# Performance work log

Measured on AMD Instinct MI355X. Metric: run time of the kernel, lower is better.

Reference implementation:

```python
import jax, jax.numpy as jnp
import numpy as np
from jax import lax

N_ROIS = 1024
ROI_H, ROI_W = 112, 224   # height divisible by 7; band = 16 rows
BANDS = 7
POOL_H, POOL_W = 8, 16    # adaptive max pool target
CONF_THRES = 0.25
PROV, ALPHA, AD = 38, 25, 35
FLAT = 16 * (POOL_H // 2) * (POOL_W // 2)  # 512 after conv+2x2 maxpool


def setup_inputs() -> dict:
    key = jax.random.key(0)
    ks = jax.random.split(key, 16)
    x = jax.random.normal(ks[0], (1, 3, 1024, 1024), dtype=jnp.float32)
    x1 = jax.random.randint(ks[1], (N_ROIS,), 0, 1024 - ROI_W)
    y1 = jax.random.randint(ks[2], (N_ROIS,), 0, 1024 - ROI_H)
    rois = jnp.stack([x1, y1, x1 + ROI_W, y1 + ROI_H], axis=-1).astype(jnp.int32)
    detection_targets = jax.random.randint(ks[3], (N_ROIS,), 0, PROV).astype(jnp.int32)
    classification_targets = jax.random.randint(ks[4], (N_ROIS, 8), 0, ALPHA).astype(jnp.int32)
    conv_w = jax.random.normal(ks[5], (16, 3, 3, 3), dtype=jnp.float32) * 0.1
    conv_b = jnp.zeros((16,), dtype=jnp.float32)
    w1 = jax.random.normal(ks[6], (8, FLAT, 128), dtype=jnp.float32) * 0.05
    b1 = jnp.zeros((8, 128), dtype=jnp.float32)
    w2_prov = jax.random.normal(ks[7], (128, PROV), dtype=jnp.float32) * 0.05
    b2_prov = jnp.zeros((PROV,), dtype=jnp.float32)
    w2_alpha = jax.random.normal(ks[8], (128, ALPHA), dtype=jnp.float32) * 0.05
    b2_alpha = jnp.zeros((ALPHA,), dtype=jnp.float32)
    w2_ad = jax.random.normal(ks[9], (6, 128, AD), dtype=jnp.float32) * 0.05
    b2_ad = jnp.zeros((6, AD), dtype=jnp.float32)
    return dict(x=x, rois=rois, detection_targets=detection_targets,
                classification_targets=classification_targets,
                conv_w=conv_w, conv_b=conv_b, w1=w1, b1=b1,
                w2_prov=w2_prov, b2_prov=b2_prov,
                w2_alpha=w2_alpha, b2_alpha=b2_alpha,
                w2_ad=w2_ad, b2_ad=b2_ad)


def _ce(logits, tgt):
    # per-row cross entropy; matches nn.CrossEntropyLoss on batch of 1 (mean==single)
    lp = jax.nn.log_softmax(logits, axis=-1)
    return -jnp.take_along_axis(lp, tgt[:, None], axis=1)[:, 0]


def _forward(x, rois, detection_targets, classification_targets,
             conv_w, conv_b, w1, b1, w2_prov, b2_prov,
             w2_alpha, b2_alpha, w2_ad, b2_ad):
    n = rois.shape[0]
    m = n * BANDS

    def extract(roi):
        return lax.dynamic_slice(x[0], (0, roi[1], roi[0]), (3, ROI_H, ROI_W))

    crops = jax.vmap(extract)(rois)                       # (N,3,112,224)
    band_h = ROI_H // BANDS                                # 16
    sub = crops.reshape(n, 3, BANDS, band_h, ROI_W)
    sub = sub.transpose(0, 2, 1, 3, 4).reshape(m, 3, band_h, ROI_W)  # (M,3,16,224)
    # adaptive max pool (16,224) -> (8,16): exact 2x14 windows
    pooled = sub.reshape(m, 3, POOL_H, band_h // POOL_H, POOL_W, ROI_W // POOL_W).max(axis=(3, 5))

    feat = lax.conv_general_dilated(pooled, conv_w, (1, 1), 'SAME',
                                    dimension_numbers=('NCHW', 'OIHW', 'NCHW'))
    feat = jax.nn.relu(feat + conv_b[None, :, None, None])  # (M,16,8,16)
    feat = feat.reshape(m, 16, POOL_H // 2, 2, POOL_W // 2, 2).max(axis=(3, 5))  # (M,16,4,8)
    flat = feat.reshape(m, FLAT)                             # (M,512)

    h = jax.nn.relu(jnp.einsum('md,kdh->kmh', flat, w1) + b1[:, None, :])  # (8,M,128)
    out_prov = h[0] @ w2_prov + b2_prov                      # (M,38)
    out_alpha = h[1] @ w2_alpha + b2_alpha                   # (M,25)
    out_ad = jnp.einsum('kmh,khc->kmc', h[2:], w2_ad) + b2_ad[:, None, :]  # (6,M,35)

    det_t = jnp.repeat(detection_targets, BANDS)             # (M,)
    det_loss = _ce(out_prov, det_t)
    mask = det_loss < CONF_THRES

    cls_t = jnp.repeat(classification_targets, BANDS, axis=0)  # (M,8)
    cls_loss = _ce(out_prov, cls_t[:, 0]) + _ce(out_alpha, cls_t[:, 1])
    cls_loss = cls_loss + jax.vmap(_ce)(out_ad, cls_t[:, 2:].T).sum(axis=0)
    total = jnp.sum(jnp.where(mask, cls_loss, 0.0))
    return out_prov, out_alpha, out_ad, mask, total


def reference(x, rois, detection_targets, classification_targets,
              conv_w, conv_b, w1, b1, w2_prov, b2_prov,
              w2_alpha, b2_alpha, w2_ad, b2_ad):
    return _forward(x, rois, detection_targets, classification_targets,
                    conv_w, conv_b, w1, b1, w2_prov, b2_prov,
                    w2_alpha, b2_alpha, w2_ad, b2_ad)
```

## Files before the change

kernel.cpp:

```cpp
#include <hip/hip_runtime.h>

#define NROIS 1024
#define BANDS 7
#define M_TOT (NROIS*BANDS)
#define ROI_W 224
#define BAND_H 16
#define FLATD 512
#define HD 1024
#define PROV 38
#define ALPHA 25
#define ADC 35
#define NAD 6

#define OFF_A     (M_TOT*PROV)
#define OFF_AD    (OFF_A + M_TOT*ALPHA)
#define OFF_MASK  (OFF_AD + NAD*M_TOT*ADC)
#define OFF_TOTAL (OFF_MASK + M_TOT)

typedef __attribute__((ext_vector_type(4))) float f32x4;
typedef __attribute__((ext_vector_type(8))) short bf16x8;

static __device__ __forceinline__ unsigned short f2bf(float f){
    union { float f; unsigned int u; } v; v.f = f;
    unsigned int u = v.u;
    unsigned int r = (u + 0x7fffu + ((u >> 16) & 1u)) >> 16;
    return (unsigned short)r;
}

#define GL16(gp, lp) __builtin_amdgcn_global_load_lds( \
    (const __attribute__((address_space(1))) unsigned int*)(gp), \
    (__attribute__((address_space(3))) unsigned int*)(lp), 16, 0, 0)

#define P2ROW(c,row) (((size_t)((c)*1023 + (row)))*1022)

__global__ __launch_bounds__(256) void k_pre_cvt(
    const float* __restrict__ x, const float* __restrict__ w1,
    const float* __restrict__ w2p, const float* __restrict__ b2p,
    const float* __restrict__ w2a, const float* __restrict__ b2a,
    const float* __restrict__ w2ad, const float* __restrict__ b2ad,
    float* __restrict__ P, unsigned short* __restrict__ Bt,
    unsigned short* __restrict__ B2, float* __restrict__ bias2)
{
    __shared__ float v[1024];
    int blk = blockIdx.x;
    int t = threadIdx.x;
    if (blk < 3069){
        int c = blk / 1023, r = blk - c*1023;
        const float* row0 = x + ((size_t)c*1024 + r)*1024;
        const float* row1 = row0 + 1024;
        #pragma unroll
        for (int i=0;i<4;i++){
            int j = t + i*256;
            v[j] = fmaxf(row0[j], row1[j]);
        }
        __syncthreads();
        float* Pr = P + P2ROW(c, r);
        #pragma unroll
        for (int i=0;i<4;i++){
            int o = t + i*256;
            if (o < 1022){
                int s = o / 73, q = o - s*73;
                int j = 14*q + s;
                if (j < 1011){
                    float mv = v[j];
                    #pragma unroll
                    for (int d=1;d<14;d++) mv = fmaxf(mv, v[j+d]);
                    Pr[o] = mv;
                }
            }
        }
    } else {
        int i = (blk - 3069)*256 + t;
        if (i < 524288){
            int k = i >> 10, n = i & 1023;
            float val = w1[((size_t)(n>>7)*512 + k)*128 + (n&127)];
            Bt[(size_t)n*512 + k] = f2bf(val);
        } else {
            int j = i - 524288;
            int h = j / 6144;
            int rem = j - h*6144;
            int n = rem >> 7, k = rem & 127;
            float val = 0.f;
            if (h == 0){ if (n < 38) val = w2p[k*38 + n]; }
            else if (h == 1){ if (n < 25) val = w2a[k*25 + n]; }
            else { if (n < 35) val = w2ad[(size_t)(h-2)*128*35 + k*35 + n]; }
            B2[j] = f2bf(val);
            if (j < 8*48){
                int hh = j / 48, nn = j - hh*48;
                float bv = 0.f;
                if (hh == 0){ if (nn < 38) bv = b2p[nn]; }
                else if (hh == 1){ if (nn < 25) bv = b2a[nn]; }
                else { if (nn < 35) bv = b2ad[(hh-2)*35 + nn]; }
                bias2[j] = bv;
            }
        }
    }
}

__global__ __launch_bounds__(256) void k_extract(
    const float* __restrict__ P, const int* __restrict__ rois,
    const float* __restrict__ conv_w, const float* __restrict__ conv_b,
    unsigned short* __restrict__ flat)
{
    __shared__ float pl[3][10][19];
    __shared__ float cw[432];
    __shared__ float cb[16];

    int blk = blockIdx.x;
    int r = blk / BANDS, b = blk - r*BANDS;
    int xx = rois[r*4+0];
    int yy = rois[r*4+1] + b*BAND_H;
    int t = threadIdx.x;
    int sx = xx % 14, qx = xx / 14;

    for (int i=t;i<432;i+=256) cw[i]=conv_w[i];
    if (t<16) cb[t]=conv_b[t];
    for (int i=t;i<3*10*19;i+=256) ((float*)pl)[i]=0.f;
    __syncthreads();

    for (int idx=t; idx<384; idx+=256){
        int c = idx>>7; int rem = idx&127; int ph = rem>>4; int pw = rem&15;
        pl[c][ph+1][pw+1] = P[P2ROW(c, yy + 2*ph) + (size_t)sx*73 + qx + pw];
    }
    __syncthreads();

    #pragma unroll
    for (int pass=0; pass<2; pass++){
        int f = t + pass*256;
        int o = f>>5, p=(f>>3)&3, q=f&7;
        float bias = cb[o];
        float s00=bias, s01=bias, s10=bias, s11=bias;
        #pragma unroll
        for (int c=0;c<3;c++){
            float w[9];
            #pragma unroll
            for (int k=0;k<9;k++) w[k] = cw[(o*3+c)*9 + k];
            float pt[4][4];
            #pragma unroll
            for (int di=0; di<4; di++)
              #pragma unroll
              for (int dj=0; dj<4; dj++)
                pt[di][dj] = pl[c][2*p+di][2*q+dj];
            #pragma unroll
            for (int kh=0;kh<3;kh++)
              #pragma unroll
              for (int kw=0;kw<3;kw++){
                float ww = w[kh*3+kw];
                s00 += pt[kh  ][kw  ]*ww;
                s01 += pt[kh  ][kw+1]*ww;
                s10 += pt[kh+1][kw  ]*ww;
                s11 += pt[kh+1][kw+1]*ww;
              }
        }
        float mx = fmaxf(fmaxf(fmaxf(s00,s01), fmaxf(s10,s11)), 0.f);
        flat[(size_t)blk*512 + f] = f2bf(mx);
    }
}

__global__ __launch_bounds__(256) void k_fc1_heads(
    const unsigned short* __restrict__ A, const unsigned short* __restrict__ Bt,
    const float* __restrict__ b1, const unsigned short* __restrict__ B2,
    const float* __restrict__ bias2, float* __restrict__ out,
    float* __restrict__ lse_ws)
{
    __shared__ short smem[16896];
    short* As = smem;
    short* Bs = smem + 8192;
    short* Hl = smem;

    int bm = blockIdx.x, h = blockIdx.y;
    int m0 = bm*128;
    int t = threadIdx.x;
    int wid = t >> 6, lane = t & 63;
    int wr = wid >> 1, wc = wid & 1;
    int l15 = lane & 15, l4 = lane >> 4;

    if (bm == 0 && h == 0 && t == 0) out[OFF_TOTAL] = 0.f;

    const unsigned short* gA = A  + ((size_t)(m0    + wid*16 + (lane>>2)))*FLATD + (lane&3)*8;
    const unsigned short* gB = Bt + ((size_t)(h*128 + wid*16 + (lane>>2)))*FLATD + (lane&3)*8;

    f32x4 acc[4][4];
    #pragma unroll
    for (int i=0;i<4;i++)
      #pragma unroll
      for (int j=0;j<4;j++) acc[i][j] = (f32x4){0.f,0.f,0.f,0.f};

    GL16(gA,            As + wid*512);
    GL16(gA + 64*FLATD, As + 2048 + wid*512);
    GL16(gB,            Bs + wid*512);
    GL16(gB + 64*FLATD, Bs + 2048 + wid*512);
    __syncthreads();

    #pragma unroll
    for (int ks=0; ks<16; ks++){
        int cur = ks & 1;
        if (ks < 15){
            int k1 = (ks+1)*32;
            int nb = (cur^1)*4096;
            GL16(gA + k1,            As + nb + wid*512);
            GL16(gA + 64*FLATD + k1, As + nb + 2048 + wid*512);
            GL16(gB + k1,            Bs + nb + wid*512);
            GL16(gB + 64*FLATD + k1, Bs + nb + 2048 + wid*512);
        }
        bf16x8 af[4], bfv[4];
        #pragma unroll
        for (int mf=0;mf<4;mf++) af[mf]  = *(const bf16x8*)&As[cur*4096 + (wr*64 + mf*16 + l15)*32 + l4*8];
        #pragma unroll
        for (int nf=0;nf<4;nf++) bfv[nf] = *(const bf16x8*)&Bs[cur*4096 + (wc*64 + nf*16 + l15)*32 + l4*8];
        #pragma unroll
        for (int mf=0;mf<4;mf++)
          #pragma unroll
          for (int nf=0;nf<4;nf++)
            acc[mf][nf] = __builtin_amdgcn_mfma_f32_16x16x32_bf16(af[mf], bfv[nf], acc[mf][nf], 0, 0, 0);
        __syncthreads();
    }

    #pragma unroll
    for (int nf=0;nf<4;nf++){
        int col = wc*64 + nf*16 + l15;
        float bias = b1[h*128 + col];
        #pragma unroll
        for (int mf=0;mf<4;mf++){
            #pragma unroll
            for (int reg=0;reg<4;reg++){
                int row = wr*64 + mf*16 + l4*4 + reg;
                Hl[row*132 + col] = (short)f2bf(fmaxf(acc[mf][nf][reg] + bias, 0.f));
            }
        }
    }
    __syncthreads();

    f32x4 acc2[2][3];
    #pragma unroll
    for (int i=0;i<2;i++)
      #pragma unroll
      for (int j=0;j<3;j++) acc2[i][j] = (f32x4){0.f,0.f,0.f,0.f};

    const unsigned short* Bh = B2 + (size_t)h*6144;
    #pragma unroll
    for (int ks=0; ks<4; ks++){
        bf16x8 ha[2], hb[3];
        #pragma unroll
        for (int m2=0;m2<2;m2++)
            ha[m2] = *(const bf16x8*)&Hl[(wid*32 + m2*16 + l15)*132 + ks*32 + l4*8];
        #pragma unroll
        for (int nf=0;nf<3;nf++)
            hb[nf] = *(const bf16x8*)(Bh + (nf*16 + l15)*128 + ks*32 + l4*8);
        #pragma unroll
        for (int m2=0;m2<2;m2++)
          #pragma unroll
          for (int nf=0;nf<3;nf++)
            acc2[m2][nf] = __builtin_amdgcn_mfma_f32_16x16x32_bf16(ha[m2], hb[nf], acc2[m2][nf], 0, 0, 0);
    }

    int Nh = (h==0) ? 38 : ((h==1) ? 25 : 35);
    #pragma unroll
    for (int nf=0;nf<3;nf++){
        int col = nf*16 + l15;
        float bv = bias2[h*48 + col];
        #pragma unroll
        for (int m2=0;m2<2;m2++){
            #pragma unroll
            for (int reg=0;reg<4;reg++){
                acc2[m2][nf][reg] += bv;
                if (col < Nh){
                    int m = m0 + wid*32 + m2*16 + l4*4 + reg;
                    size_t a;
                    if (h == 0)      a = (size_t)m*38 + col;
                    else if (h == 1) a = OFF_A + (size_t)m*25 + col;
                    else             a = OFF_AD + ((size_t)(h-2)*M_TOT + m)*35 + col;
                    out[a] = acc2[m2][nf][reg];
                }
            }
        }
    }

    #pragma unroll
    for (int m2=0;m2<2;m2++){
        #pragma unroll
        for (int reg=0;reg<4;reg++){
            float mx = -1e30f;
            #pragma unroll
            for (int nf=0;nf<3;nf++){
                int col = nf*16 + l15;
                if (col < Nh) mx = fmaxf(mx, acc2[m2][nf][reg]);
            }
            #pragma unroll
            for (int d=1; d<16; d<<=1) mx = fmaxf(mx, __shfl_xor(mx, d));
            float s = 0.f;
            #pragma unroll
            for (int nf=0;nf<3;nf++){
                int col = nf*16 + l15;
                if (col < Nh) s += __expf(acc2[m2][nf][reg] - mx);
            }
            #pragma unroll
            for (int d=1; d<16; d<<=1) s += __shfl_xor(s, d);
            if (l15 == 0){
                int m = m0 + wid*32 + m2*16 + l4*4 + reg;
                lse_ws[(size_t)m*8 + h] = mx + __logf(s);
            }
        }
    }
}

__global__ __launch_bounds__(256) void k_loss(
    const float* __restrict__ lse_ws, const int* __restrict__ det_t,
    const int* __restrict__ cls_t, float* __restrict__ out)
{
    int m = blockIdx.x*256 + threadIdx.x;
    if (m >= M_TOT) return;
    int r = m / 7;
    const float* L = lse_ws + (size_t)m*8;
    float det_loss = L[0] - out[(size_t)m*38 + det_t[r]];
    bool mk = det_loss < 0.25f;
    out[OFF_MASK + m] = mk ? 1.f : 0.f;
    if (mk){
        const int* ct = cls_t + r*8;
        float c = (L[0] - out[(size_t)m*38 + ct[0]]) + (L[1] - out[OFF_A + (size_t)m*25 + ct[1]]);
        #pragma unroll
        for (int j=0;j<6;j++)
            c += L[2+j] - out[OFF_AD + ((size_t)j*M_TOT + m)*35 + ct[2+j]];
        atomicAdd(out + OFF_TOTAL, c);
    }
}

extern "C" void kernel_launch(void* const* d_in, const int* in_sizes, int n_in,
                              void* d_out, int out_size, void* d_ws, size_t ws_size,
                              hipStream_t stream) {
    const float* x      = (const float*)d_in[0];
    const int*   rois   = (const int*)d_in[1];
    const int*   det    = (const int*)d_in[2];
    const int*   cls    = (const int*)d_in[3];
    const float* conv_w = (const float*)d_in[4];
    const float* conv_b = (const float*)d_in[5];
    const float* w1     = (const float*)d_in[6];
    const float* b1     = (const float*)d_in[7];
    const float* w2p    = (const float*)d_in[8];
    const float* b2p    = (const float*)d_in[9];
    const float* w2a    = (const float*)d_in[10];
    const float* b2a    = (const float*)d_in[11];
    const float* w2ad   = (const float*)d_in[12];
    const float* b2ad   = (const float*)d_in[13];
    float* out = (float*)d_out;

    char* w = (char*)d_ws;
    unsigned short* flatbf = (unsigned short*)w;
    unsigned short* BtW    = (unsigned short*)(w + 7340032);
    unsigned short* B2     = (unsigned short*)(w + 8388608);
    float*  bias2          = (float*)(w + 8486912);
    float*  lse            = (float*)(w + 8488448);
    float*  P              = (float*)(w + 8717824);

    k_pre_cvt<<<3069 + 2240, 256, 0, stream>>>(x, w1, w2p, b2p, w2a, b2a, w2ad, b2ad,
                                               P, BtW, B2, bias2);
    k_extract<<<M_TOT, 256, 0, stream>>>(P, rois, conv_w, conv_b, flatbf);
    k_fc1_heads<<<dim3(56, 8), 256, 0, stream>>>(flatbf, BtW, b1, B2, bias2, out, lse);
    k_loss<<<28, 256, 0, stream>>>(lse, det, cls, out);
}
```

Baseline: 151.7 us.

## Process all seven bands per block in extract kernel with register-held weights

The extract kernel now launches one block per ROI instead of one per band and loops over the seven bands inside the block. Conv weights for two output channels are loaded into registers once per thread and reused across bands, which amortizes the weight, bias and zero-fill setup. The LDS tile row is padded to 20 so the patch can be read with 2-wide vector loads. The cost is fewer blocks (1024 instead of 7168), more registers per thread, and a serial band loop with two barriers per iteration, which could reduce latency hiding.

```diff
diff --git a/kernel.cpp b/kernel.cpp
--- a/kernel.cpp
+++ b/kernel.cpp
@@ -18,6 +18,7 @@
 #define OFF_TOTAL (OFF_MASK + M_TOT)
 
 typedef __attribute__((ext_vector_type(4))) float f32x4;
+typedef __attribute__((ext_vector_type(2))) float f32x2;
 typedef __attribute__((ext_vector_type(8))) short bf16x8;
 
 static __device__ __forceinline__ unsigned short f2bf(float f){
@@ -102,58 +103,70 @@
     const float* __restrict__ conv_w, const float* __restrict__ conv_b,
     unsigned short* __restrict__ flat)
 {
-    __shared__ float pl[3][10][19];
+    __shared__ float pl[3][10][20];
     __shared__ float cw[432];
     __shared__ float cb[16];
 
-    int blk = blockIdx.x;
-    int r = blk / BANDS, b = blk - r*BANDS;
+    int r = blockIdx.x;
+    int t = threadIdx.x;
     int xx = rois[r*4+0];
-    int yy = rois[r*4+1] + b*BAND_H;
-    int t = threadIdx.x;
+    int y1 = rois[r*4+1];
     int sx = xx % 14, qx = xx / 14;
+    int o2 = t >> 5, p = (t >> 3) & 3, q = t & 7;
 
     for (int i=t;i<432;i+=256) cw[i]=conv_w[i];
     if (t<16) cb[t]=conv_b[t];
-    for (int i=t;i<3*10*19;i+=256) ((float*)pl)[i]=0.f;
+    for (int i=t;i<3*10*20;i+=256) ((float*)pl)[i]=0.f;
     __syncthreads();
 
-    for (int idx=t; idx<384; idx+=256){
-        int c = idx>>7; int rem = idx&127; int ph = rem>>4; int pw = rem&15;
-        pl[c][ph+1][pw+1] = P[P2ROW(c, yy + 2*ph) + (size_t)sx*73 + qx + pw];
-    }
-    __syncthreads();
-
-    #pragma unroll
-    for (int pass=0; pass<2; pass++){
-        int f = t + pass*256;
-        int o = f>>5, p=(f>>3)&3, q=f&7;
-        float bias = cb[o];
-        float s00=bias, s01=bias, s10=bias, s11=bias;
+    float w[2][27];
+    #pragma unroll
+    for (int oi=0;oi<2;oi++){
+        int o = o2 + oi*8;
+        #pragma unroll
+        for (int k=0;k<27;k++) w[oi][k] = cw[o*27 + k];
+    }
+    float bias0 = cb[o2], bias1 = cb[o2+8];
+
+    for (int b=0; b<BANDS; b++){
+        int yy = y1 + b*BAND_H;
+        for (int idx=t; idx<384; idx+=256){
+            int c = idx>>7; int rem = idx&127; int ph = rem>>4; int pw = rem&15;
+            pl[c][ph+1][pw+1] = P[P2ROW(c, yy + 2*ph) + (size_t)sx*73 + qx + pw];
+        }
+        __syncthreads();
+
+        float s0[4] = {bias0,bias0,bias0,bias0};
+        float s1[4] = {bias1,bias1,bias1,bias1};
         #pragma unroll
         for (int c=0;c<3;c++){
-            float w[9];
-            #pragma unroll
-            for (int k=0;k<9;k++) w[k] = cw[(o*3+c)*9 + k];
             float pt[4][4];
             #pragma unroll
-            for (int di=0; di<4; di++)
-              #pragma unroll
-              for (int dj=0; dj<4; dj++)
-                pt[di][dj] = pl[c][2*p+di][2*q+dj];
+            for (int di=0; di<4; di++){
+                f32x2 a = *(const f32x2*)&pl[c][2*p+di][2*q];
+                f32x2 bb = *(const f32x2*)&pl[c][2*p+di][2*q+2];
+                pt[di][0]=a.x; pt[di][1]=a.y; pt[di][2]=bb.x; pt[di][3]=bb.y;
+            }
             #pragma unroll
             for (int kh=0;kh<3;kh++)
               #pragma unroll
               for (int kw=0;kw<3;kw++){
-                float ww = w[kh*3+kw];
-                s00 += pt[kh  ][kw  ]*ww;
-                s01 += pt[kh  ][kw+1]*ww;
-                s10 += pt[kh+1][kw  ]*ww;
-                s11 += pt[kh+1][kw+1]*ww;
+                float w0 = w[0][c*9+kh*3+kw];
+                float w1v = w[1][c*9+kh*3+kw];
+                #pragma unroll
+                for (int pos=0;pos<4;pos++){
+                    float pv = pt[kh + (pos>>1)][kw + (pos&1)];
+                    s0[pos] += pv*w0;
+                    s1[pos] += pv*w1v;
+                }
               }
         }
-        float mx = fmaxf(fmaxf(fmaxf(s00,s01), fmaxf(s10,s11)), 0.f);
-        flat[(size_t)blk*512 + f] = f2bf(mx);
+        float mx0 = fmaxf(fmaxf(fmaxf(s0[0],s0[1]), fmaxf(s0[2],s0[3])), 0.f);
+        float mx1 = fmaxf(fmaxf(fmaxf(s1[0],s1[1]), fmaxf(s1[2],s1[3])), 0.f);
+        size_t base = ((size_t)r*BANDS + b)*512;
+        flat[base + t]       = f2bf(mx0);
+        flat[base + t + 256] = f2bf(mx1);
+        __syncthreads();
     }
 }
 
@@ -354,7 +367,7 @@
 
     k_pre_cvt<<<3069 + 2240, 256, 0, stream>>>(x, w1, w2p, b2p, w2a, b2a, w2ad, b2ad,
                                                P, BtW, B2, bias2);
-    k_extract<<<M_TOT, 256, 0, stream>>>(P, rois, conv_w, conv_b, flatbf);
+    k_extract<<<NROIS, 256, 0, stream>>>(P, rois, conv_w, conv_b, flatbf);
     k_fc1_heads<<<dim3(56, 8), 256, 0, stream>>>(flatbf, BtW, b1, B2, bias2, out, lse);
     k_loss<<<28, 256, 0, stream>>>(lse, det, cls, out);
 }
```

New measurement: 134.0 us. 11.7% less time.
